# Optimization experiments

Measured on AMD Instinct MI355X. Metric: run time of the kernel, lower is better.

Reference implementation:

```python
import jax, jax.numpy as jnp
import numpy as np

BS, SEQ, H, OUT = 32, 64, 256, 1

def setup_inputs() -> dict:
    key = jax.random.key(0)
    ks = jax.random.split(key, 8)
    s3 = 1.0 / np.sqrt(3 * H)
    sh = 1.0 / np.sqrt(H)
    x = jax.random.normal(ks[0], (BS, SEQ, H), dtype=jnp.float32)
    # ChaoticAttention: Linear(3H -> H) scoring, softmax over seq
    Wa = jax.random.normal(ks[1], (3 * H, H), dtype=jnp.float32) * s3
    ba = jnp.zeros((H,), dtype=jnp.float32)
    # ChaoticLSTM cell: gates = context @ Wi + ht @ Wh + b, order i,f,g,o
    Wi = jax.random.normal(ks[2], (H, 4 * H), dtype=jnp.float32) * sh
    Wh = jax.random.normal(ks[3], (H, 4 * H), dtype=jnp.float32) * sh
    b = jnp.zeros((4 * H,), dtype=jnp.float32)
    # final fc: Linear(H -> OUT)
    Wf = jax.random.normal(ks[4], (H, OUT), dtype=jnp.float32) * sh
    bf = jnp.zeros((OUT,), dtype=jnp.float32)
    return {"x": x, "Wa": Wa, "ba": ba, "Wi": Wi, "Wh": Wh, "b": b, "Wf": Wf, "bf": bf}

def reference(x, Wa, ba, Wi, Wh, b, Wf, bf):
    bs, seq, hid = x.shape

    def step(carry, _):
        ht, ct = carry
        # attention over the full input sequence conditioned on (ht, ct)
        hrep = jnp.broadcast_to(ht[:, None, :], (bs, seq, hid))
        crep = jnp.broadcast_to(ct[:, None, :], (bs, seq, hid))
        feat = jnp.concatenate([x, hrep, crep], axis=-1)          # (bs, seq, 3H)
        alpha = jax.nn.softmax(feat @ Wa + ba, axis=1)            # softmax over seq
        context = jnp.sum(alpha * x, axis=1)                      # (bs, H)
        # one LSTM cell step on the context vector
        gates = context @ Wi + ht @ Wh + b                        # (bs, 4H)
        i, f, g, o = jnp.split(gates, 4, axis=-1)
        ct_new = jax.nn.sigmoid(f) * ct + jax.nn.sigmoid(i) * jnp.tanh(g)
        ht_new = jax.nn.sigmoid(o) * jnp.tanh(ct_new)
        return (ht_new, ct_new), None

    h0 = jnp.zeros((bs, hid), dtype=x.dtype)
    c0 = jnp.zeros((bs, hid), dtype=x.dtype)
    (ht, ct), _ = jax.lax.scan(step, (h0, c0), None, length=seq)
    return ht @ Wf + bf                                           # (bs, OUT)
```

## Files before the change

### kernel.cpp

```cpp
#include <hip/hip_runtime.h>

#define BSZ   32
#define SEQ   64
#define HID   256
#define G4    1024
#define NSTEP 64
#define QB    8
#define JB    32

typedef unsigned long long u64;
typedef unsigned int       u32;

__device__ __forceinline__ float sigmoidf_(float v) { return 1.f / (1.f + __expf(-v)); }

__global__ __launch_bounds__(256, 1) void k_fused(
    const float* __restrict__ x, const float* __restrict__ Wa,
    const float* __restrict__ Wi, const float* __restrict__ Wh,
    const float* __restrict__ bias, const float* __restrict__ Wf,
    const float* __restrict__ bf,
    u64* __restrict__ tht, u64* __restrict__ ctxT, float* __restrict__ out)
{
  const int b    = blockIdx.x & 31;
  const int q    = blockIdx.x >> 5;
  const int tid  = threadIdx.x;
  const int lane = tid & 63;
  const int wv   = tid >> 6;
  const int jq   = tid & 7;
  const int g    = (tid >> 3) & 3;
  const int kq   = tid >> 5;

  __shared__ __align__(16) float arena[32768];
  __shared__ __align__(16) float hs[256];
  __shared__ __align__(16) float cs[256];
  __shared__ __align__(16) float gred[2][8][JB * 4];
  __shared__ float red[4];

  const float* xb = x + (size_t)b * SEQ * HID;

#pragma unroll
  for (int it = 0; it < 16; ++it) {
    const int gl = it * 1024 + tid * 4;
    const int s = gl >> 8, k = gl & 255;
    *(float4*)&arena[s * 260 + k] = *(const float4*)(xb + gl);
  }
#pragma unroll
  for (int it = 0; it < 8; ++it) {
    const int idx = it * 256 + tid;
    const int k = idx >> 3, cq = idx & 7;
    *(float4*)&arena[16640 + k * 32 + cq * 4] =
        *(const float4*)(Wa + (size_t)k * HID + q * JB + cq * 4);
  }
  __syncthreads();

  {
    const int ts = tid >> 2, tc = tid & 3;
    float l0 = 0.f, l1 = 0.f, l2 = 0.f, l3 = 0.f,
          l4 = 0.f, l5 = 0.f, l6 = 0.f, l7 = 0.f;
    const float* xrow = &arena[ts * 260];
    const float* wab  = &arena[16640 + tc * 8];
    for (int k4 = 0; k4 < 64; ++k4) {
      const float4 xv = *(const float4*)&xrow[k4 * 4];
#define LSTEP(XE, KO)                                                        \
      { const float4 wa = *(const float4*)&wab[(k4 * 4 + KO) * 32];          \
        const float4 wb2 = *(const float4*)&wab[(k4 * 4 + KO) * 32 + 4];     \
        l0 += (XE) * wa.x;  l1 += (XE) * wa.y;  l2 += (XE) * wa.z;           \
        l3 += (XE) * wa.w;  l4 += (XE) * wb2.x; l5 += (XE) * wb2.y;          \
        l6 += (XE) * wb2.z; l7 += (XE) * wb2.w; }
      LSTEP(xv.x, 0) LSTEP(xv.y, 1) LSTEP(xv.z, 2) LSTEP(xv.w, 3)
#undef LSTEP
    }
    float* lrow = &arena[24832 + ts * 33 + tc * 8];
    lrow[0] = l0; lrow[1] = l1; lrow[2] = l2; lrow[3] = l3;
    lrow[4] = l4; lrow[5] = l5; lrow[6] = l6; lrow[7] = l7;
  }
  __syncthreads();

  {
    const int jx = tid >> 3, sp = tid & 7;
    float lg[8];
#pragma unroll
    for (int e = 0; e < 8; ++e) lg[e] = arena[24832 + (sp * 8 + e) * 33 + jx];
    float m = lg[0];
#pragma unroll
    for (int e = 1; e < 8; ++e) m = fmaxf(m, lg[e]);
    m = fmaxf(m, __shfl_xor(m, 1));
    m = fmaxf(m, __shfl_xor(m, 2));
    m = fmaxf(m, __shfl_xor(m, 4));
    float ex[8], sm = 0.f;
#pragma unroll
    for (int e = 0; e < 8; ++e) { ex[e] = __expf(lg[e] - m); sm += ex[e]; }
    sm += __shfl_xor(sm, 1);
    sm += __shfl_xor(sm, 2);
    sm += __shfl_xor(sm, 4);
    const float inv = 1.f / sm;
    const int gj = q * JB + jx;
    float cx = 0.f;
#pragma unroll
    for (int e = 0; e < 8; ++e) cx += ex[e] * arena[(sp * 8 + e) * 260 + gj];
    cx *= inv;
    cx += __shfl_xor(cx, 1);
    cx += __shfl_xor(cx, 2);
    cx += __shfl_xor(cx, 4);
    if (sp == 0)
      __hip_atomic_store(ctxT + b * HID + gj,
                         (((u64)__float_as_uint(cx)) << 32) | 1ull,
                         __ATOMIC_RELAXED, __HIP_MEMORY_SCOPE_AGENT);
  }
  __syncthreads();

#define MAC32(HSRC, ACC)                                                     \
  _Pragma("unroll")                                                          \
  for (int k4 = 0; k4 < 8; ++k4) {                                           \
    const float4 h4 = *(const float4*)&(HSRC)[kq * 32 + k4 * 4];             \
    const float* wp = &arena[(kq * 32 + k4 * 4) * 128 + g * 32 + jq * 4];    \
    const float4 w0 = *(const float4*)&wp[0];                                \
    const float4 w1 = *(const float4*)&wp[128];                              \
    const float4 w2 = *(const float4*)&wp[256];                              \
    const float4 w3 = *(const float4*)&wp[384];                              \
    ACC.x += h4.x * w0.x + h4.y * w1.x + h4.z * w2.x + h4.w * w3.x;          \
    ACC.y += h4.x * w0.y + h4.y * w1.y + h4.z * w2.y + h4.w * w3.y;          \
    ACC.z += h4.x * w0.z + h4.y * w1.z + h4.z * w2.z + h4.w * w3.z;          \
    ACC.w += h4.x * w0.w + h4.y * w1.w + h4.z * w2.w + h4.w * w3.w;          \
  }

#pragma unroll
  for (int i = 0; i < 32; ++i) {
    const int f = i * 256 + tid;
    const int k = f >> 5, c4 = f & 31;
    const int gq = c4 >> 3, jw = c4 & 7;
    *(float4*)&arena[f * 4] =
        *(const float4*)(Wi + (size_t)k * G4 + gq * HID + q * JB + jw * 4);
  }
  {
    const u64* pp = ctxT + b * HID + tid;
    u64 pk;
    do {
      pk = __hip_atomic_load(pp, __ATOMIC_RELAXED, __HIP_MEMORY_SCOPE_AGENT);
    } while ((u32)pk != 1u);
    cs[tid] = __uint_as_float((u32)(pk >> 32));
  }
  __syncthreads();

  float4 ac = {0.f, 0.f, 0.f, 0.f};
  MAC32(cs, ac);
  *(float4*)&gred[0][kq][g * 32 + jq * 4] = ac;
  __syncthreads();

  float4 gcr = {0.f, 0.f, 0.f, 0.f};
  float  cst = 0.f;
  if (tid < 32) {
    const int qj = q * JB + tid;
#pragma unroll
    for (int k2 = 0; k2 < 8; ++k2) {
      const float* gp = &gred[0][k2][tid];
      gcr.x += gp[0]; gcr.y += gp[32]; gcr.z += gp[64]; gcr.w += gp[96];
    }
    gcr.x += bias[qj];           gcr.y += bias[HID + qj];
    gcr.z += bias[2 * HID + qj]; gcr.w += bias[3 * HID + qj];
    const float ig = sigmoidf_(gcr.x);
    const float gg = tanhf(gcr.z), og = sigmoidf_(gcr.w);
    cst = ig * gg;
    const float hv = og * tanhf(cst);
    __hip_atomic_store(tht + (size_t)1 * BSZ * HID + (size_t)b * HID + qj,
                       (((u64)__float_as_uint(hv)) << 32) | 1ull,
                       __ATOMIC_RELAXED, __HIP_MEMORY_SCOPE_AGENT);
  }
#pragma unroll
  for (int i = 0; i < 32; ++i) {
    const int f = i * 256 + tid;
    const int k = f >> 5, c4 = f & 31;
    const int gq = c4 >> 3, jw = c4 & 7;
    *(float4*)&arena[f * 4] =
        *(const float4*)(Wh + (size_t)k * G4 + gq * HID + q * JB + jw * 4);
  }
  __syncthreads();

  for (int t = 1; t < NSTEP; ++t) {
    const int rb = t & 1;
    {
      const u64* pp = tht + (size_t)rb * BSZ * HID + (size_t)b * HID + tid;
      u64 pk;
      do {
        pk = __hip_atomic_load(pp, __ATOMIC_RELAXED, __HIP_MEMORY_SCOPE_AGENT);
      } while ((u32)pk != (u32)t);
      hs[tid] = __uint_as_float((u32)(pk >> 32));
    }
    float4 a2 = {0.f, 0.f, 0.f, 0.f};
    MAC32(hs, a2);
    *(float4*)&gred[rb][kq][g * 32 + jq * 4] = a2;
    __syncthreads();

    if (tid < 32) {
      float4 s = gcr;
#pragma unroll
      for (int k2 = 0; k2 < 8; ++k2) {
        const float* gp = &gred[rb][k2][tid];
        s.x += gp[0]; s.y += gp[32]; s.z += gp[64]; s.w += gp[96];
      }
      const float ig = sigmoidf_(s.x), fg = sigmoidf_(s.y);
      const float gg = tanhf(s.z),     og = sigmoidf_(s.w);
      cst = fg * cst + ig * gg;
      const float hv = og * tanhf(cst);
      __hip_atomic_store(tht + (size_t)((t + 1) & 1) * BSZ * HID
                             + (size_t)b * HID + q * JB + tid,
                         (((u64)__float_as_uint(hv)) << 32) | (u64)(u32)(t + 1),
                         __ATOMIC_RELAXED, __HIP_MEMORY_SCOPE_AGENT);
    }
  }

  if (q == 0) {
    const u64* pp = tht +  (size_t)b * HID + tid;
    u64 pk;
    do {
      pk = __hip_atomic_load(pp, __ATOMIC_RELAXED, __HIP_MEMORY_SCOPE_AGENT);
    } while ((u32)pk != (u32)NSTEP);
    const float hv = __uint_as_float((u32)(pk >> 32));
    float prod = hv * Wf[tid];
#pragma unroll
    for (int mk = 1; mk < 64; mk <<= 1) prod += __shfl_xor(prod, mk);
    if (lane == 0) red[wv] = prod;
    __syncthreads();
    if (tid == 0) out[b] = red[0] + red[1] + red[2] + red[3] + bf[0];
  }
#undef MAC32
}

extern "C" void kernel_launch(void* const* d_in, const int* in_sizes, int n_in,
                              void* d_out, int out_size, void* d_ws, size_t ws_size,
                              hipStream_t stream)
{
  const float* x  = (const float*)d_in[0];
  const float* Wa = (const float*)d_in[1];
  const float* Wi = (const float*)d_in[3];
  const float* Wh = (const float*)d_in[4];
  const float* bi = (const float*)d_in[5];
  const float* Wf = (const float*)d_in[6];
  const float* bf = (const float*)d_in[7];
  float* out = (float*)d_out;

  u64* tht  = (u64*)d_ws;
  u64* ctxT = (u64*)((char*)d_ws + 2 * BSZ * HID * sizeof(u64));

  hipLaunchKernelGGL(k_fused, dim3(BSZ * QB), dim3(256), 0, stream,
                     x, Wa, Wi, Wh, bi, Wf, bf, tht, ctxT, out);
}
```

Baseline: 159.2 us.

## Split hidden units across 16 blocks per batch with two blocks per CU

Each block now owns 16 hidden units instead of 32, doubling the grid to 512 persistent blocks. The shared-memory footprint is cut by tiling the attention-logit GEMM over k, and by re-reading x from global memory for the context sum, so two blocks fit per CU. This halves the per-step Wh multiply-accumulate and the gate reduction work on the serial recurrence path. In exchange there are twice as many blocks polling the shared h buffer each step. The spin-wait scheme now depends on all 512 blocks being co-resident, which holds only if each CU actually fits two blocks.

```diff
diff --git a/kernel.cpp b/kernel.cpp
--- a/kernel.cpp
+++ b/kernel.cpp
@@ -5,15 +5,15 @@
 #define HID   256
 #define G4    1024
 #define NSTEP 64
-#define QB    8
-#define JB    32
+#define QB    16
+#define JB    16
 
 typedef unsigned long long u64;
 typedef unsigned int       u32;
 
 __device__ __forceinline__ float sigmoidf_(float v) { return 1.f / (1.f + __expf(-v)); }
 
-__global__ __launch_bounds__(256, 1) void k_fused(
+__global__ __launch_bounds__(256, 2) void k_fused(
     const float* __restrict__ x, const float* __restrict__ Wa,
     const float* __restrict__ Wi, const float* __restrict__ Wh,
     const float* __restrict__ bias, const float* __restrict__ Wf,
@@ -25,82 +25,80 @@
   const int tid  = threadIdx.x;
   const int lane = tid & 63;
   const int wv   = tid >> 6;
-  const int jq   = tid & 7;
-  const int g    = (tid >> 3) & 3;
-  const int kq   = tid >> 5;
-
-  __shared__ __align__(16) float arena[32768];
-  __shared__ __align__(16) float hs[256];
-  __shared__ __align__(16) float cs[256];
-  __shared__ __align__(16) float gred[2][8][JB * 4];
+  const int cq   = tid & 15;
+  const int kq   = tid >> 4;
+
+  __shared__ __align__(16) float arena[18944];
   __shared__ float red[4];
+  float* xs   = arena;
+  float* was  = arena + 4352;
+  float* Ls   = arena + 5376;
+  float* hs   = arena + 16384;
+  float* cs   = arena + 16640;
+  float* gred = arena + 16896;
 
   const float* xb = x + (size_t)b * SEQ * HID;
 
-#pragma unroll
-  for (int it = 0; it < 16; ++it) {
-    const int gl = it * 1024 + tid * 4;
-    const int s = gl >> 8, k = gl & 255;
-    *(float4*)&arena[s * 260 + k] = *(const float4*)(xb + gl);
-  }
-#pragma unroll
-  for (int it = 0; it < 8; ++it) {
-    const int idx = it * 256 + tid;
-    const int k = idx >> 3, cq = idx & 7;
-    *(float4*)&arena[16640 + k * 32 + cq * 4] =
-        *(const float4*)(Wa + (size_t)k * HID + q * JB + cq * 4);
-  }
-  __syncthreads();
-
+  float l0 = 0.f, l1 = 0.f, l2 = 0.f, l3 = 0.f;
+  const int ts = tid >> 2, tc = tid & 3;
+  for (int kt = 0; kt < 4; ++kt) {
+    __syncthreads();
+#pragma unroll
+    for (int i = 0; i < 4; ++i) {
+      const int f = i * 256 + tid;
+      const int s = f >> 4, kc = (f & 15) * 4;
+      *(float4*)&xs[s * 68 + kc] = *(const float4*)(xb + s * HID + kt * 64 + kc);
+    }
+    {
+      const int k = tid >> 2, jw = tid & 3;
+      *(float4*)&was[k * 16 + jw * 4] =
+          *(const float4*)(Wa + (size_t)(kt * 64 + k) * HID + q * JB + jw * 4);
+    }
+    __syncthreads();
+#pragma unroll
+    for (int k4 = 0; k4 < 16; ++k4) {
+      const float4 xv = *(const float4*)&xs[ts * 68 + k4 * 4];
+#pragma unroll
+      for (int e = 0; e < 4; ++e) {
+        const float xe = (e == 0) ? xv.x : (e == 1) ? xv.y : (e == 2) ? xv.z : xv.w;
+        const float4 w4 = *(const float4*)&was[(k4 * 4 + e) * 16 + tc * 4];
+        l0 += xe * w4.x; l1 += xe * w4.y; l2 += xe * w4.z; l3 += xe * w4.w;
+      }
+    }
+  }
   {
-    const int ts = tid >> 2, tc = tid & 3;
-    float l0 = 0.f, l1 = 0.f, l2 = 0.f, l3 = 0.f,
-          l4 = 0.f, l5 = 0.f, l6 = 0.f, l7 = 0.f;
-    const float* xrow = &arena[ts * 260];
-    const float* wab  = &arena[16640 + tc * 8];
-    for (int k4 = 0; k4 < 64; ++k4) {
-      const float4 xv = *(const float4*)&xrow[k4 * 4];
-#define LSTEP(XE, KO)                                                        \
-      { const float4 wa = *(const float4*)&wab[(k4 * 4 + KO) * 32];          \
-        const float4 wb2 = *(const float4*)&wab[(k4 * 4 + KO) * 32 + 4];     \
-        l0 += (XE) * wa.x;  l1 += (XE) * wa.y;  l2 += (XE) * wa.z;           \
-        l3 += (XE) * wa.w;  l4 += (XE) * wb2.x; l5 += (XE) * wb2.y;          \
-        l6 += (XE) * wb2.z; l7 += (XE) * wb2.w; }
-      LSTEP(xv.x, 0) LSTEP(xv.y, 1) LSTEP(xv.z, 2) LSTEP(xv.w, 3)
-#undef LSTEP
-    }
-    float* lrow = &arena[24832 + ts * 33 + tc * 8];
-    lrow[0] = l0; lrow[1] = l1; lrow[2] = l2; lrow[3] = l3;
-    lrow[4] = l4; lrow[5] = l5; lrow[6] = l6; lrow[7] = l7;
+    float* lr = &Ls[ts * 20 + tc * 4];
+    lr[0] = l0; lr[1] = l1; lr[2] = l2; lr[3] = l3;
   }
   __syncthreads();
 
   {
-    const int jx = tid >> 3, sp = tid & 7;
-    float lg[8];
-#pragma unroll
-    for (int e = 0; e < 8; ++e) lg[e] = arena[24832 + (sp * 8 + e) * 33 + jx];
-    float m = lg[0];
-#pragma unroll
-    for (int e = 1; e < 8; ++e) m = fmaxf(m, lg[e]);
+    const int jx = tid >> 4, sp = tid & 15;
+    float lg[4];
+#pragma unroll
+    for (int e = 0; e < 4; ++e) lg[e] = Ls[(sp * 4 + e) * 20 + jx];
+    float m = fmaxf(fmaxf(lg[0], lg[1]), fmaxf(lg[2], lg[3]));
     m = fmaxf(m, __shfl_xor(m, 1));
     m = fmaxf(m, __shfl_xor(m, 2));
     m = fmaxf(m, __shfl_xor(m, 4));
-    float ex[8], sm = 0.f;
-#pragma unroll
-    for (int e = 0; e < 8; ++e) { ex[e] = __expf(lg[e] - m); sm += ex[e]; }
+    m = fmaxf(m, __shfl_xor(m, 8));
+    float ex[4], sm = 0.f;
+#pragma unroll
+    for (int e = 0; e < 4; ++e) { ex[e] = __expf(lg[e] - m); sm += ex[e]; }
     sm += __shfl_xor(sm, 1);
     sm += __shfl_xor(sm, 2);
     sm += __shfl_xor(sm, 4);
+    sm += __shfl_xor(sm, 8);
     const float inv = 1.f / sm;
     const int gj = q * JB + jx;
     float cx = 0.f;
 #pragma unroll
-    for (int e = 0; e < 8; ++e) cx += ex[e] * arena[(sp * 8 + e) * 260 + gj];
+    for (int e = 0; e < 4; ++e) cx += ex[e] * xb[(sp * 4 + e) * HID + gj];
     cx *= inv;
     cx += __shfl_xor(cx, 1);
     cx += __shfl_xor(cx, 2);
     cx += __shfl_xor(cx, 4);
+    cx += __shfl_xor(cx, 8);
     if (sp == 0)
       __hip_atomic_store(ctxT + b * HID + gj,
                          (((u64)__float_as_uint(cx)) << 32) | 1ull,
@@ -108,15 +106,15 @@
   }
   __syncthreads();
 
-#define MAC32(HSRC, ACC)                                                     \
+#define MAC16(HSRC, ACC)                                                     \
   _Pragma("unroll")                                                          \
-  for (int k4 = 0; k4 < 8; ++k4) {                                           \
-    const float4 h4 = *(const float4*)&(HSRC)[kq * 32 + k4 * 4];             \
-    const float* wp = &arena[(kq * 32 + k4 * 4) * 128 + g * 32 + jq * 4];    \
+  for (int k4 = 0; k4 < 4; ++k4) {                                           \
+    const float4 h4 = *(const float4*)&(HSRC)[kq * 16 + k4 * 4];             \
+    const float* wp = &arena[(kq * 16 + k4 * 4) * 64 + cq * 4];              \
     const float4 w0 = *(const float4*)&wp[0];                                \
-    const float4 w1 = *(const float4*)&wp[128];                              \
-    const float4 w2 = *(const float4*)&wp[256];                              \
-    const float4 w3 = *(const float4*)&wp[384];                              \
+    const float4 w1 = *(const float4*)&wp[64];                               \
+    const float4 w2 = *(const float4*)&wp[128];                              \
+    const float4 w3 = *(const float4*)&wp[192];                              \
     ACC.x += h4.x * w0.x + h4.y * w1.x + h4.z * w2.x + h4.w * w3.x;          \
     ACC.y += h4.x * w0.y + h4.y * w1.y + h4.z * w2.y + h4.w * w3.y;          \
     ACC.z += h4.x * w0.z + h4.y * w1.z + h4.z * w2.z + h4.w * w3.z;          \
@@ -124,12 +122,11 @@
   }
 
 #pragma unroll
-  for (int i = 0; i < 32; ++i) {
+  for (int i = 0; i < 16; ++i) {
     const int f = i * 256 + tid;
-    const int k = f >> 5, c4 = f & 31;
-    const int gq = c4 >> 3, jw = c4 & 7;
+    const int k = f >> 4, c4 = f & 15, gg = c4 >> 2, jw = c4 & 3;
     *(float4*)&arena[f * 4] =
-        *(const float4*)(Wi + (size_t)k * G4 + gq * HID + q * JB + jw * 4);
+        *(const float4*)(Wi + (size_t)k * G4 + gg * HID + q * JB + jw * 4);
   }
   {
     const u64* pp = ctxT + b * HID + tid;
@@ -142,36 +139,32 @@
   __syncthreads();
 
   float4 ac = {0.f, 0.f, 0.f, 0.f};
-  MAC32(cs, ac);
-  *(float4*)&gred[0][kq][g * 32 + jq * 4] = ac;
-  __syncthreads();
-
-  float4 gcr = {0.f, 0.f, 0.f, 0.f};
-  float  cst = 0.f;
-  if (tid < 32) {
-    const int qj = q * JB + tid;
-#pragma unroll
-    for (int k2 = 0; k2 < 8; ++k2) {
-      const float* gp = &gred[0][k2][tid];
-      gcr.x += gp[0]; gcr.y += gp[32]; gcr.z += gp[64]; gcr.w += gp[96];
-    }
-    gcr.x += bias[qj];           gcr.y += bias[HID + qj];
-    gcr.z += bias[2 * HID + qj]; gcr.w += bias[3 * HID + qj];
-    const float ig = sigmoidf_(gcr.x);
-    const float gg = tanhf(gcr.z), og = sigmoidf_(gcr.w);
-    cst = ig * gg;
-    const float hv = og * tanhf(cst);
-    __hip_atomic_store(tht + (size_t)1 * BSZ * HID + (size_t)b * HID + qj,
-                       (((u64)__float_as_uint(hv)) << 32) | 1ull,
-                       __ATOMIC_RELAXED, __HIP_MEMORY_SCOPE_AGENT);
-  }
-#pragma unroll
-  for (int i = 0; i < 32; ++i) {
+  MAC16(cs, ac);
+  *(float4*)&gred[kq * 64 + cq * 4] = ac;
+  __syncthreads();
+
+  float gc = 0.f, cst = 0.f;
+  if (wv == 0) {
+#pragma unroll
+    for (int k2 = 0; k2 < 16; ++k2) gc += gred[k2 * 64 + lane];
+    gc += bias[(lane >> 4) * HID + q * JB + (lane & 15)];
+    const float gx2 = __shfl_xor(gc, 32), ox = __shfl_xor(gc, 48);
+    if (lane < 16) {
+      const float ig = sigmoidf_(gc);
+      const float g2 = tanhf(gx2), og = sigmoidf_(ox);
+      cst = ig * g2;
+      const float hv = og * tanhf(cst);
+      __hip_atomic_store(tht + (size_t)BSZ * HID + (size_t)b * HID + q * JB + lane,
+                         (((u64)__float_as_uint(hv)) << 32) | 1ull,
+                         __ATOMIC_RELAXED, __HIP_MEMORY_SCOPE_AGENT);
+    }
+  }
+#pragma unroll
+  for (int i = 0; i < 16; ++i) {
     const int f = i * 256 + tid;
-    const int k = f >> 5, c4 = f & 31;
-    const int gq = c4 >> 3, jw = c4 & 7;
+    const int k = f >> 4, c4 = f & 15, gg = c4 >> 2, jw = c4 & 3;
     *(float4*)&arena[f * 4] =
-        *(const float4*)(Wh + (size_t)k * G4 + gq * HID + q * JB + jw * 4);
+        *(const float4*)(Wh + (size_t)k * G4 + gg * HID + q * JB + jw * 4);
   }
   __syncthreads();
 
@@ -186,25 +179,27 @@
       hs[tid] = __uint_as_float((u32)(pk >> 32));
     }
     float4 a2 = {0.f, 0.f, 0.f, 0.f};
-    MAC32(hs, a2);
-    *(float4*)&gred[rb][kq][g * 32 + jq * 4] = a2;
-    __syncthreads();
-
-    if (tid < 32) {
-      float4 s = gcr;
-#pragma unroll
-      for (int k2 = 0; k2 < 8; ++k2) {
-        const float* gp = &gred[rb][k2][tid];
-        s.x += gp[0]; s.y += gp[32]; s.z += gp[64]; s.w += gp[96];
+    MAC16(hs, a2);
+    *(float4*)&gred[rb * 1024 + kq * 64 + cq * 4] = a2;
+    __syncthreads();
+
+    if (wv == 0) {
+      float s_ = gc;
+#pragma unroll
+      for (int k2 = 0; k2 < 16; ++k2) s_ += gred[rb * 1024 + k2 * 64 + lane];
+      const float fx  = __shfl_xor(s_, 16);
+      const float gx2 = __shfl_xor(s_, 32);
+      const float ox  = __shfl_xor(s_, 48);
+      if (lane < 16) {
+        const float ig = sigmoidf_(s_), fg = sigmoidf_(fx);
+        const float g2 = tanhf(gx2),    og = sigmoidf_(ox);
+        cst = fg * cst + ig * g2;
+        const float hv = og * tanhf(cst);
+        __hip_atomic_store(tht + (size_t)((t + 1) & 1) * BSZ * HID
+                               + (size_t)b * HID + q * JB + lane,
+                           (((u64)__float_as_uint(hv)) << 32) | (u64)(u32)(t + 1),
+                           __ATOMIC_RELAXED, __HIP_MEMORY_SCOPE_AGENT);
       }
-      const float ig = sigmoidf_(s.x), fg = sigmoidf_(s.y);
-      const float gg = tanhf(s.z),     og = sigmoidf_(s.w);
-      cst = fg * cst + ig * gg;
-      const float hv = og * tanhf(cst);
-      __hip_atomic_store(tht + (size_t)((t + 1) & 1) * BSZ * HID
-                             + (size_t)b * HID + q * JB + tid,
-                         (((u64)__float_as_uint(hv)) << 32) | (u64)(u32)(t + 1),
-                         __ATOMIC_RELAXED, __HIP_MEMORY_SCOPE_AGENT);
     }
   }
 
@@ -222,7 +217,7 @@
     __syncthreads();
     if (tid == 0) out[b] = red[0] + red[1] + red[2] + red[3] + bf[0];
   }
-#undef MAC32
+#undef MAC16
 }
 
 extern "C" void kernel_launch(void* const* d_in, const int* in_sizes, int n_in,
```

Measured after the change: 171.5 us. +7.7%, slower.

## Store recurrent weights and hidden state as packed fp16 and use dot2

Applied to the files above, without the earlier changes.

The Wi/Wh slices held in LDS are converted to packed fp16 pairs, and the recurrent matvec uses fdot2 instructions on packed fp16 hidden-state values instead of fp32 FMAs. The hidden state exchanged between blocks through global atomics is also packed two values per slot, which halves the number of polled words per step. Sigmoid and tanh switch to fast exp-based versions. This cuts LDS traffic, ALU work and cross-block exchange volume on the serial 64-step critical path, at the cost of fp16 rounding in the recurrent weights, context and hidden state.

```diff
diff --git a/kernel.cpp b/kernel.cpp
--- a/kernel.cpp
+++ b/kernel.cpp
@@ -10,15 +10,35 @@
 
 typedef unsigned long long u64;
 typedef unsigned int       u32;
-
-__device__ __forceinline__ float sigmoidf_(float v) { return 1.f / (1.f + __expf(-v)); }
+typedef _Float16 h2v __attribute__((ext_vector_type(2)));
+
+__device__ __forceinline__ u32 pk2(float lo, float hi) {
+  return __builtin_bit_cast(u32, __builtin_amdgcn_cvt_pkrtz(lo, hi));
+}
+__device__ __forceinline__ float dot2_(u32 w, u32 h, float acc) {
+#if __has_builtin(__builtin_amdgcn_fdot2)
+  return __builtin_amdgcn_fdot2(__builtin_bit_cast(h2v, w),
+                                __builtin_bit_cast(h2v, h), acc, false);
+#else
+  const h2v wv = __builtin_bit_cast(h2v, w), hv = __builtin_bit_cast(h2v, h);
+  return acc + (float)wv[0] * (float)hv[0] + (float)wv[1] * (float)hv[1];
+#endif
+}
+__device__ __forceinline__ float sigmoid_f(float x) {
+  return __fdividef(1.f, 1.f + __expf(-x));
+}
+__device__ __forceinline__ float tanh_f(float x) {
+  const float xc = fminf(fmaxf(x, -18.f), 18.f);
+  const float e  = __expf(2.f * xc);
+  return __fdividef(e - 1.f, e + 1.f);
+}
 
 __global__ __launch_bounds__(256, 1) void k_fused(
     const float* __restrict__ x, const float* __restrict__ Wa,
     const float* __restrict__ Wi, const float* __restrict__ Wh,
     const float* __restrict__ bias, const float* __restrict__ Wf,
     const float* __restrict__ bf,
-    u64* __restrict__ tht, u64* __restrict__ ctxT, float* __restrict__ out)
+    u64* __restrict__ tht2, u64* __restrict__ ctxT, float* __restrict__ out)
 {
   const int b    = blockIdx.x & 31;
   const int q    = blockIdx.x >> 5;
@@ -28,12 +48,15 @@
   const int jq   = tid & 7;
   const int g    = (tid >> 3) & 3;
   const int kq   = tid >> 5;
-
-  __shared__ __align__(16) float arena[32768];
-  __shared__ __align__(16) float hs[256];
+  const int cq4  = g * 8 + jq;
+
+  __shared__ __align__(16) u32   smem[26944];
+  __shared__ __align__(16) u32   hs2[128];
   __shared__ __align__(16) float cs[256];
-  __shared__ __align__(16) float gred[2][8][JB * 4];
+  __shared__ __align__(16) float gred[2][8][128];
   __shared__ float red[4];
+  float* arena = (float*)smem;
+  u32*   lds_w = smem;
 
   const float* xb = x + (size_t)b * SEQ * HID;
 
@@ -108,29 +131,31 @@
   }
   __syncthreads();
 
-#define MAC32(HSRC, ACC)                                                     \
+#define STAGE_W16(SRC)                                                       \
   _Pragma("unroll")                                                          \
-  for (int k4 = 0; k4 < 8; ++k4) {                                           \
-    const float4 h4 = *(const float4*)&(HSRC)[kq * 32 + k4 * 4];             \
-    const float* wp = &arena[(kq * 32 + k4 * 4) * 128 + g * 32 + jq * 4];    \
-    const float4 w0 = *(const float4*)&wp[0];                                \
-    const float4 w1 = *(const float4*)&wp[128];                              \
-    const float4 w2 = *(const float4*)&wp[256];                              \
-    const float4 w3 = *(const float4*)&wp[384];                              \
-    ACC.x += h4.x * w0.x + h4.y * w1.x + h4.z * w2.x + h4.w * w3.x;          \
-    ACC.y += h4.x * w0.y + h4.y * w1.y + h4.z * w2.y + h4.w * w3.y;          \
-    ACC.z += h4.x * w0.z + h4.y * w1.z + h4.z * w2.z + h4.w * w3.z;          \
-    ACC.w += h4.x * w0.w + h4.y * w1.w + h4.z * w2.w + h4.w * w3.w;          \
-  }
-
-#pragma unroll
-  for (int i = 0; i < 32; ++i) {
-    const int f = i * 256 + tid;
-    const int k = f >> 5, c4 = f & 31;
-    const int gq = c4 >> 3, jw = c4 & 7;
-    *(float4*)&arena[f * 4] =
-        *(const float4*)(Wi + (size_t)k * G4 + gq * HID + q * JB + jw * 4);
-  }
+  for (int i = 0; i < 16; ++i) {                                             \
+    const int idx = i * 256 + tid;                                           \
+    const int kp = idx >> 5, c4 = idx & 31;                                  \
+    const int gc = (c4 >> 3) * HID + q * JB + (c4 & 7) * 4;                  \
+    const float4 a  = *(const float4*)((SRC) + (size_t)(2 * kp) * G4 + gc);  \
+    const float4 b2 = *(const float4*)((SRC) + (size_t)(2 * kp + 1) * G4 + gc);\
+    *(uint4*)&lds_w[kp * 128 + c4 * 4] =                                     \
+        make_uint4(pk2(a.x, b2.x), pk2(a.y, b2.y),                           \
+                   pk2(a.z, b2.z), pk2(a.w, b2.w));                          \
+  }
+
+#define MACW(H2SRC, ACC)                                                     \
+  _Pragma("unroll")                                                          \
+  for (int kpl = 0; kpl < 16; ++kpl) {                                       \
+    const uint4 wq = *(const uint4*)&lds_w[(kq * 16 + kpl) * 128 + cq4 * 4]; \
+    const u32 h2 = (H2SRC)[kpl];                                             \
+    ACC.x = dot2_(wq.x, h2, ACC.x);                                          \
+    ACC.y = dot2_(wq.y, h2, ACC.y);                                          \
+    ACC.z = dot2_(wq.z, h2, ACC.z);                                          \
+    ACC.w = dot2_(wq.w, h2, ACC.w);                                          \
+  }
+
+  STAGE_W16(Wi)
   {
     const u64* pp = ctxT + b * HID + tid;
     u64 pk;
@@ -141,9 +166,15 @@
   }
   __syncthreads();
 
-  float4 ac = {0.f, 0.f, 0.f, 0.f};
-  MAC32(cs, ac);
-  *(float4*)&gred[0][kq][g * 32 + jq * 4] = ac;
+  {
+    u32 ch2[16];
+    const float2* cp = (const float2*)&cs[kq * 32];
+#pragma unroll
+    for (int i = 0; i < 16; ++i) ch2[i] = pk2(cp[i].x, cp[i].y);
+    float4 ac = {0.f, 0.f, 0.f, 0.f};
+    MACW(ch2, ac)
+    *(float4*)&gred[0][kq][cq4 * 4] = ac;
+  }
   __syncthreads();
 
   float4 gcr = {0.f, 0.f, 0.f, 0.f};
@@ -157,37 +188,44 @@
     }
     gcr.x += bias[qj];           gcr.y += bias[HID + qj];
     gcr.z += bias[2 * HID + qj]; gcr.w += bias[3 * HID + qj];
-    const float ig = sigmoidf_(gcr.x);
-    const float gg = tanhf(gcr.z), og = sigmoidf_(gcr.w);
-    cst = ig * gg;
-    const float hv = og * tanhf(cst);
-    __hip_atomic_store(tht + (size_t)1 * BSZ * HID + (size_t)b * HID + qj,
-                       (((u64)__float_as_uint(hv)) << 32) | 1ull,
-                       __ATOMIC_RELAXED, __HIP_MEMORY_SCOPE_AGENT);
-  }
-#pragma unroll
-  for (int i = 0; i < 32; ++i) {
-    const int f = i * 256 + tid;
-    const int k = f >> 5, c4 = f & 31;
-    const int gq = c4 >> 3, jw = c4 & 7;
-    *(float4*)&arena[f * 4] =
-        *(const float4*)(Wh + (size_t)k * G4 + gq * HID + q * JB + jw * 4);
-  }
+    const float ig = sigmoid_f(gcr.x);
+    const float g2 = tanh_f(gcr.z), og = sigmoid_f(gcr.w);
+    cst = ig * g2;
+    const float hv = og * tanh_f(cst);
+    const float hp_ = __shfl_xor(hv, 1);
+    if ((tid & 1) == 0) {
+      const u32 d = pk2(hv, hp_);
+      __hip_atomic_store(tht2 + (size_t)BSZ * 128 + b * 128 + q * 16 + (tid >> 1),
+                         (((u64)d) << 32) | 1ull,
+                         __ATOMIC_RELAXED, __HIP_MEMORY_SCOPE_AGENT);
+    }
+  }
+  STAGE_W16(Wh)
   __syncthreads();
 
   for (int t = 1; t < NSTEP; ++t) {
     const int rb = t & 1;
     {
-      const u64* pp = tht + (size_t)rb * BSZ * HID + (size_t)b * HID + tid;
+      const u64* pp = tht2 + (size_t)rb * BSZ * 128 + b * 128 + (tid >> 1);
       u64 pk;
       do {
         pk = __hip_atomic_load(pp, __ATOMIC_RELAXED, __HIP_MEMORY_SCOPE_AGENT);
       } while ((u32)pk != (u32)t);
-      hs[tid] = __uint_as_float((u32)(pk >> 32));
+      hs2[tid >> 1] = (u32)(pk >> 32);
     }
     float4 a2 = {0.f, 0.f, 0.f, 0.f};
-    MAC32(hs, a2);
-    *(float4*)&gred[rb][kq][g * 32 + jq * 4] = a2;
+    {
+      const u32* hp = &hs2[kq * 16];
+      u32 hh[16];
+#pragma unroll
+      for (int i4 = 0; i4 < 4; ++i4) {
+        const uint4 hq = *(const uint4*)&hp[i4 * 4];
+        hh[i4 * 4 + 0] = hq.x; hh[i4 * 4 + 1] = hq.y;
+        hh[i4 * 4 + 2] = hq.z; hh[i4 * 4 + 3] = hq.w;
+      }
+      MACW(hh, a2)
+    }
+    *(float4*)&gred[rb][kq][cq4 * 4] = a2;
     __syncthreads();
 
     if (tid < 32) {
@@ -197,32 +235,38 @@
         const float* gp = &gred[rb][k2][tid];
         s.x += gp[0]; s.y += gp[32]; s.z += gp[64]; s.w += gp[96];
       }
-      const float ig = sigmoidf_(s.x), fg = sigmoidf_(s.y);
-      const float gg = tanhf(s.z),     og = sigmoidf_(s.w);
-      cst = fg * cst + ig * gg;
-      const float hv = og * tanhf(cst);
-      __hip_atomic_store(tht + (size_t)((t + 1) & 1) * BSZ * HID
-                             + (size_t)b * HID + q * JB + tid,
-                         (((u64)__float_as_uint(hv)) << 32) | (u64)(u32)(t + 1),
-                         __ATOMIC_RELAXED, __HIP_MEMORY_SCOPE_AGENT);
+      const float ig = sigmoid_f(s.x), fg = sigmoid_f(s.y);
+      const float g2 = tanh_f(s.z),    og = sigmoid_f(s.w);
+      cst = fg * cst + ig * g2;
+      const float hv = og * tanh_f(cst);
+      const float hp_ = __shfl_xor(hv, 1);
+      if ((tid & 1) == 0) {
+        const u32 d = pk2(hv, hp_);
+        __hip_atomic_store(tht2 + (size_t)((t + 1) & 1) * BSZ * 128
+                               + b * 128 + q * 16 + (tid >> 1),
+                           (((u64)d) << 32) | (u64)(u32)(t + 1),
+                           __ATOMIC_RELAXED, __HIP_MEMORY_SCOPE_AGENT);
+      }
     }
   }
 
   if (q == 0) {
-    const u64* pp = tht +  (size_t)b * HID + tid;
+    const u64* pp = tht2 +  b * 128 + (tid >> 1);
     u64 pk;
     do {
       pk = __hip_atomic_load(pp, __ATOMIC_RELAXED, __HIP_MEMORY_SCOPE_AGENT);
     } while ((u32)pk != (u32)NSTEP);
-    const float hv = __uint_as_float((u32)(pk >> 32));
-    float prod = hv * Wf[tid];
+    const h2v hh = __builtin_bit_cast(h2v, (u32)(pk >> 32));
+    const float hval = (tid & 1) ? (float)hh[1] : (float)hh[0];
+    float prod = hval * Wf[tid];
 #pragma unroll
     for (int mk = 1; mk < 64; mk <<= 1) prod += __shfl_xor(prod, mk);
     if (lane == 0) red[wv] = prod;
     __syncthreads();
     if (tid == 0) out[b] = red[0] + red[1] + red[2] + red[3] + bf[0];
   }
-#undef MAC32
+#undef MACW
+#undef STAGE_W16
 }
 
 extern "C" void kernel_launch(void* const* d_in, const int* in_sizes, int n_in,
@@ -238,9 +282,9 @@
   const float* bf = (const float*)d_in[7];
   float* out = (float*)d_out;
 
-  u64* tht  = (u64*)d_ws;
-  u64* ctxT = (u64*)((char*)d_ws + 2 * BSZ * HID * sizeof(u64));
+  u64* tht2 = (u64*)d_ws;
+  u64* ctxT = (u64*)((char*)d_ws + (size_t)2 * BSZ * 128 * sizeof(u64));
 
   hipLaunchKernelGGL(k_fused, dim3(BSZ * QB), dim3(256), 0, stream,
-                     x, Wa, Wi, Wh, bi, Wf, bf, tht, ctxT, out);
-}
+                     x, Wa, Wi, Wh, bi, Wf, bf, tht2, ctxT, out);
+}
```

Result: slower. 179.2 us (+12.6%).
